# Performance work log

Measured on AMD Instinct MI355X. Metric: run time of the kernel, lower is better.

Reference implementation:

```python
import jax, jax.numpy as jnp
import numpy as np

N_NODES = 16
N_EDGES = 64
N_LAYERS = 4


def _gcn(x, src, dst, emask, W, b):
    # PyG GCNConv: add self-loops, symmetric deg^-1/2 normalization, sum-aggregate.
    n = x.shape[0]
    h = x @ W  # [n, d_out]
    deg = jax.ops.segment_sum(emask, dst, num_segments=n) + 1.0  # +1 self-loop
    dinv = jax.lax.rsqrt(deg)
    norm = dinv[src] * dinv[dst] * emask  # masked-out edges get 0 weight
    out = jax.ops.segment_sum(norm[:, None] * h[src], dst, num_segments=n)
    return out + (dinv * dinv)[:, None] * h + b  # self-loop term + bias


def _sag_pool(x, src, dst, emask, w_rel, b_rel, w_root, k):
    # SAGPooling with GraphConv scorer: score = lin_rel(sum_j x_j) + lin_root(x)
    n = x.shape[0]
    agg = jax.ops.segment_sum(emask[:, None] * x[src], dst, num_segments=n)
    score = agg @ w_rel + b_rel + x @ w_root  # [n]
    perm = jnp.argsort(-score)[:k]  # top-k nodes
    x_new = x[perm] * jnp.tanh(score[perm])[:, None]
    kept = jnp.zeros(n, bool).at[perm].set(True)
    pos = jnp.zeros(n, jnp.int32).at[perm].set(jnp.arange(k, dtype=jnp.int32))
    emask_new = emask * kept[src] * kept[dst]  # drop edges touching removed nodes
    return x_new, pos[src], pos[dst], emask_new


def _conv_gnn(x, src, dst, W0, Ws, bs, pWrel, pbrel, pWroot, linW, linb):
    emask = jnp.ones(src.shape[0], x.dtype)
    n = x.shape[0]
    for i in range(N_LAYERS):
        W = W0 if i == 0 else Ws[i - 1]
        x = jax.nn.relu(_gcn(x, src, dst, emask, W, bs[i]))
        k = -(-n // 2)  # ceil(0.5 * n) -- SAGPooling ratio=0.5
        x, src, dst, emask = _sag_pool(x, src, dst, emask, pWrel[i], pbrel[i], pWroot[i], k)
        n = k
    x = x @ linW + linb  # [1, 128]
    return jax.nn.log_softmax(x, axis=1)


def _fc(h, fcW, fcb, lnw, lnb):
    eps = 1e-5
    for i in range(3):
        h = h @ fcW[i] + fcb[i]
        mu = h.mean(-1, keepdims=True)
        var = ((h - mu) ** 2).mean(-1, keepdims=True)
        h = (h - mu) * jax.lax.rsqrt(var + eps) * lnw[i] + lnb[i]
        h = jax.nn.relu(h)
    return h @ fcW[3] + fcb[3]


def setup_inputs() -> dict:
    key = jax.random.key(0)
    ks = iter(jax.random.split(key, 64))

    def rn(shape, s=0.05):
        return jax.random.normal(next(ks), shape, jnp.float32) * s

    def gnn_params(p):
        return {
            p + '_W0': rn((45, 128)), p + '_W': rn((3, 128, 128)),
            p + '_b': jnp.zeros((4, 128), jnp.float32),
            p + '_pWrel': rn((4, 128)), p + '_pbrel': jnp.zeros((4,), jnp.float32),
            p + '_pWroot': rn((4, 128)),
            p + '_linW': rn((128, 128)), p + '_linb': jnp.zeros((128,), jnp.float32),
        }

    inp = {
        'gp_x': rn((N_NODES, 45), 1.0), 'sp_x': rn((N_NODES, 45), 1.0),
        'gp_src': jax.random.randint(next(ks), (N_EDGES,), 0, N_NODES, jnp.int32),
        'gp_dst': jax.random.randint(next(ks), (N_EDGES,), 0, N_NODES, jnp.int32),
        'sp_src': jax.random.randint(next(ks), (N_EDGES,), 0, N_NODES, jnp.int32),
        'sp_dst': jax.random.randint(next(ks), (N_EDGES,), 0, N_NODES, jnp.int32),
        'fcW': rn((4, 256, 256)), 'fcb': jnp.zeros((4, 256), jnp.float32),
        'lnw': jnp.ones((3, 256), jnp.float32), 'lnb': jnp.zeros((3, 256), jnp.float32),
    }
    inp.update(gnn_params('g'))
    inp.update(gnn_params('s'))
    return inp


def reference(gp_x, sp_x, gp_src, gp_dst, sp_src, sp_dst,
              g_W0, g_W, g_b, g_pWrel, g_pbrel, g_pWroot, g_linW, g_linb,
              s_W0, s_W, s_b, s_pWrel, s_pbrel, s_pWroot, s_linW, s_linb,
              fcW, fcb, lnw, lnb):
    out1 = _conv_gnn(gp_x, gp_src, gp_dst, g_W0, g_W, g_b, g_pWrel, g_pbrel, g_pWroot, g_linW, g_linb)
    out2 = _conv_gnn(sp_x, sp_src, sp_dst, s_W0, s_W, s_b, s_pWrel, s_pbrel, s_pWroot, s_linW, s_linb)
    concat = jnp.concatenate((out1.reshape(-1), out2.reshape(-1)))  # [256]
    return _fc(concat, fcW, fcb, lnw, lnb)
```

## Files before the change

### kernel.cpp

```cpp
#include <hip/hip_runtime.h>
#include <math.h>

#define MAGIC 0x5F3759DFu
typedef unsigned int u32;

__device__ __forceinline__ void bar_lds(){
  asm volatile("s_waitcnt lgkmcnt(0)\n\ts_barrier" ::: "memory");
}
__device__ __forceinline__ void bar_vm0(){
  asm volatile("s_waitcnt vmcnt(0) lgkmcnt(0)\n\ts_barrier" ::: "memory");
}
__device__ __forceinline__ void bar_vm8(){
  asm volatile("s_waitcnt vmcnt(8) lgkmcnt(0)\n\ts_barrier" ::: "memory");
}

__device__ inline float wsum(float v){
  #pragma unroll
  for (int o=32;o;o>>=1) v += __shfl_xor(v,o,64);
  return v;
}
__device__ inline float wmax(float v){
  #pragma unroll
  for (int o=32;o;o>>=1) v = fmaxf(v,__shfl_xor(v,o,64));
  return v;
}
__device__ inline float hsum32(float v){
  #pragma unroll
  for (int o=16;o;o>>=1) v += __shfl_xor(v,o,64);
  return v;
}
__device__ __forceinline__ void stageW(const float* g, float* l, int nfloats,
                                       int wid, int lane){
  const int nch = nfloats>>8;
  for (int c=wid; c<nch; c+=8)
    __builtin_amdgcn_global_load_lds(
      (__attribute__((address_space(1))) u32*)(void*)(g+(c<<8)+(lane<<2)),
      (__attribute__((address_space(3))) u32*)(void*)(l+(c<<8)), 16, 0, 0);
}
__device__ __forceinline__ void pf(const float* p, int nfloats, int tid){
  float4 acc={0.f,0.f,0.f,0.f};
  const int nq=nfloats>>2;
  for (int i=tid;i<nq;i+=512){
    const float4 v=((const float4*)p)[i];
    acc.x+=v.x; acc.y+=v.y; acc.z+=v.z; acc.w+=v.w;
  }
  asm volatile("" :: "v"(acc.x),"v"(acc.y),"v"(acc.z),"v"(acc.w));
}
__device__ __forceinline__ void poll1(const u32* f, int lane){
  u32 v=0;
  do {
    if (lane==0) v=__hip_atomic_load(f,__ATOMIC_ACQUIRE,__HIP_MEMORY_SCOPE_AGENT);
    v=(u32)__shfl((int)v,0,64);
    if (v!=MAGIC) __builtin_amdgcn_s_sleep(1);
  } while (v!=MAGIC);
}
__device__ __forceinline__ float aload(const float* p){
  return __hip_atomic_load(p,__ATOMIC_RELAXED,__HIP_MEMORY_SCOPE_AGENT);
}
__device__ __forceinline__ void astore(float* p, float v){
  __hip_atomic_store(p,v,__ATOMIC_RELAXED,__HIP_MEMORY_SCOPE_AGENT);
}

template<int F,int VH,int N>
__device__ __forceinline__ void cmain2(int lt, const float* slot,
                                       const float* ZBp, float* PBp){
  constexpr int CH = 128/F;
  const int c4 = lt&31, r = lt>>5;
  const int fh = r & (F-1), vh = r / F;
  const int f0 = fh*CH;
  const float4* slot4 = (const float4*)slot;
  float4 acc[VH];
  #pragma unroll
  for (int i=0;i<VH;++i) acc[i]=make_float4(0.f,0.f,0.f,0.f);
  #pragma unroll
  for (int f=0; f<CH; ++f){
    const float4 w4 = slot4[(f0+f)*32 + c4];
    #pragma unroll
    for (int i=0;i<VH;++i){
      const float zv = ZBp[((vh*VH+i)<<7) + f0 + f];
      acc[i].x+=zv*w4.x; acc[i].y+=zv*w4.y; acc[i].z+=zv*w4.z; acc[i].w+=zv*w4.w;
    }
  }
  #pragma unroll
  for (int i=0;i<VH;++i){
    acc[i].x+=__shfl_xor(acc[i].x,32,64);
    acc[i].y+=__shfl_xor(acc[i].y,32,64);
    acc[i].z+=__shfl_xor(acc[i].z,32,64);
    acc[i].w+=__shfl_xor(acc[i].w,32,64);
  }
  if (!(r&1)){
    const int fp = fh>>1;
    float4* P4=(float4*)PBp;
    #pragma unroll
    for (int i=0;i<VH;++i)
      P4[(fp*N + vh*VH + i)*32 + c4] = acc[i];
  }
}

__global__ __launch_bounds__(512,1) void net_kernel(
    const float* __restrict__ gp_x, const float* __restrict__ sp_x,
    const int* __restrict__ gp_src, const int* __restrict__ gp_dst,
    const int* __restrict__ sp_src, const int* __restrict__ sp_dst,
    const float* __restrict__ g_W0, const float* __restrict__ g_W,
    const float* __restrict__ g_b,  const float* __restrict__ g_pWrel,
    const float* __restrict__ g_pbrel, const float* __restrict__ g_pWroot,
    const float* __restrict__ g_linW, const float* __restrict__ g_linb,
    const float* __restrict__ s_W0, const float* __restrict__ s_W,
    const float* __restrict__ s_b,  const float* __restrict__ s_pWrel,
    const float* __restrict__ s_pbrel, const float* __restrict__ s_pWroot,
    const float* __restrict__ s_linW, const float* __restrict__ s_linb,
    const float* __restrict__ fcW, const float* __restrict__ fcb,
    const float* __restrict__ lnw, const float* __restrict__ lnb,
    float* __restrict__ wsbuf, float* __restrict__ out)
{
  __shared__ __align__(16) float slotA[16384];
  __shared__ __align__(16) float slotB[16384];
  __shared__ __align__(16) float XBx[16][128];
  __shared__ __align__(16) float ZBraw[1024];
  __shared__ __align__(16) float PBf[2048];
  __shared__ __align__(16) float wrelL[512], wrootL[512];
  __shared__ __align__(16) float Adn[256], Mdn[256];
  __shared__ float d1P[64], d2P[64];
  __shared__ float yA[128];
  __shared__ float tsA[8]; __shared__ int permA[8];
  __shared__ float fcin[256]; __shared__ float wpart[16];

  const int lt  = threadIdx.x;
  const int bid = blockIdx.x;
  const int wid = lt>>6, lane = lt&63;

  if (bid >= 6){
    if (bid==6){ pf(g_W0,5760,lt); pf(g_pWrel,512,lt); pf(g_pWroot,512,lt);
                 pf(g_b,512,lt);   pf(g_linb,128,lt); }
    else if (bid==7){ pf(s_W0,5760,lt); pf(s_pWrel,512,lt); pf(s_pWroot,512,lt);
                 pf(s_b,512,lt);   pf(s_linb,128,lt); }
    else if (bid<=11) pf(g_W + (bid-8)*12288, 12288, lt);
    else if (bid<=15) pf(s_W + (bid-12)*12288, 12288, lt);
    else if (bid<=17) pf(g_linW + (bid-16)*8192, 8192, lt);
    else              pf(s_linW + (bid-18)*8192, 8192, lt);
    return;
  }

  if (bid >= 2){
    const int L = bid-2;
    const int qfc=(wid<<3)+(lane&7), f0fc=(lane>>3)<<5;
    float4 wr[32];
    #pragma unroll
    for (int t=0;t<32;++t) wr[t]=*(const float4*)(fcW+(L<<16)+(f0fc+t)*256+(qfc<<2));
    const float4 bb=*(const float4*)(fcb+(L<<8)+(qfc<<2));
    float4 lw={0,0,0,0}, lb2={0,0,0,0};
    if (L<3){ lw=*(const float4*)(lnw+(L<<8)+(qfc<<2)); lb2=*(const float4*)(lnb+(L<<8)+(qfc<<2)); }

    float zr[32];
    if (L==0){
      poll1((const u32*)(wsbuf+128), lane);
      poll1((const u32*)(wsbuf+384), lane);
      if (lt<256){
        const float* src = wsbuf + (lt<128 ? lt : 128+lt);
        fcin[lt]=aload(src);
      }
      bar_lds();
      #pragma unroll
      for (int t=0;t<32;++t) zr[t]=fcin[f0fc+t];
    } else {
      const int floff = (L==1)?768 : (L==2)?1280 : 1792;
      const int srcoff= (L==1)?512 : (L==2)?1024 : 1536;
      poll1((const u32*)(wsbuf+floff), lane);
      #pragma unroll
      for (int t=0;t<32;++t) zr[t]=aload(wsbuf+srcoff+f0fc+t);
    }
    float4 a={0.f,0.f,0.f,0.f};
    #pragma unroll
    for (int t=0;t<32;++t){
      a.x+=zr[t]*wr[t].x; a.y+=zr[t]*wr[t].y; a.z+=zr[t]*wr[t].z; a.w+=zr[t]*wr[t].w;
    }
    #pragma unroll
    for (int m=8;m<64;m<<=1){
      a.x+=__shfl_xor(a.x,m,64); a.y+=__shfl_xor(a.y,m,64);
      a.z+=__shfl_xor(a.z,m,64); a.w+=__shfl_xor(a.w,m,64);
    }
    if (L==3){
      if (lane<8){
        float4 r; r.x=a.x+bb.x; r.y=a.y+bb.y; r.z=a.z+bb.z; r.w=a.w+bb.w;
        *(float4*)(out+(qfc<<2))=r;
      }
      return;
    }
    const bool act=(lane<8);
    float4 hv={0.f,0.f,0.f,0.f};
    if (act){
      hv.x=a.x+bb.x; hv.y=a.y+bb.y; hv.z=a.z+bb.z; hv.w=a.w+bb.w;
      float s=hv.x+hv.y+hv.z+hv.w;
      float s2=hv.x*hv.x+hv.y*hv.y+hv.z*hv.z+hv.w*hv.w;
      #pragma unroll
      for (int m=1;m<8;m<<=1){ s+=__shfl_xor(s,m,64); s2+=__shfl_xor(s2,m,64); }
      if (lane==0){ wpart[wid]=s; wpart[8+wid]=s2; }
    }
    bar_lds();
    if (act){
      float S=0.f,S2=0.f;
      #pragma unroll
      for (int w2=0;w2<8;++w2){ S+=wpart[w2]; S2+=wpart[8+w2]; }
      const float mu=S*(1.f/256.f);
      const float ri=rsqrtf(S2*(1.f/256.f)-mu*mu+1e-5f);
      float* dst=wsbuf+512+L*512+(qfc<<2);
      astore(dst+0,fmaxf((hv.x-mu)*ri*lw.x+lb2.x,0.f));
      astore(dst+1,fmaxf((hv.y-mu)*ri*lw.y+lb2.y,0.f));
      astore(dst+2,fmaxf((hv.z-mu)*ri*lw.z+lb2.z,0.f));
      astore(dst+3,fmaxf((hv.w-mu)*ri*lw.w+lb2.w,0.f));
    }
    bar_vm0();
    if (lt==0) __hip_atomic_store((u32*)(wsbuf+512+L*512+256),MAGIC,__ATOMIC_RELEASE,__HIP_MEMORY_SCOPE_AGENT);
    return;
  }

  const int br = bid;
  const float* x0    = br ? sp_x    : gp_x;
  const int*   srcg  = br ? sp_src  : gp_src;
  const int*   dstg  = br ? sp_dst  : gp_dst;
  const float* W0    = br ? s_W0    : g_W0;
  const float* Wl    = br ? s_W     : g_W;
  const float* bl    = br ? s_b     : g_b;
  const float* wrel  = br ? s_pWrel : g_pWrel;
  const float* brel  = br ? s_pbrel : g_pbrel;
  const float* wroot = br ? s_pWroot: g_pWroot;
  const float* linWg = br ? s_linW  : g_linW;
  const float* linb  = br ? s_linb  : g_linb;
  float* wsOut = wsbuf + br*256;
  u32*   wsFlag = (u32*)(wsbuf + 128 + br*256);

  float xv[4];
  #pragma unroll
  for (int r=0;r<4;++r){
    const int i=lt+(r<<9), v=i>>7, f=i&127;
    xv[r] = (f<45)? x0[v*45+f] : 0.f;
  }
  int es=0, ed=0; float emk=0.f;
  if (lt<64){ es=srcg[lt]; ed=dstg[lt]; emk=1.f; }
  const float4 brelv = *(const float4*)brel;
  const int bi4=(lt&31)<<2;
  const float4 blv0=*(const float4*)(bl       + bi4);
  const float4 blv1=*(const float4*)(bl + 128 + bi4);
  const float4 blv2=*(const float4*)(bl + 256 + bi4);
  const float4 blv3=*(const float4*)(bl + 384 + bi4);
  const float linb_s = linb[lt>>2];
  asm volatile("" ::: "memory");
  stageW(wrel,  wrelL,  512, wid, lane);
  stageW(wroot, wrootL, 512, wid, lane);
  stageW(Wl,    slotA, 16384, wid, lane);

  auto build_dense=[&](int kk, float wlane, bool with_ts){
    const float4 z4={0.f,0.f,0.f,0.f};
    *(float4*)&Adn[lt<<2]=z4;
    *(float4*)&Mdn[lt<<2]=z4;
    const bool act=(emk!=0.f);
    int mycnt=0;
    for (int v=0;v<kk;++v){
      const unsigned long long m=__ballot(act&&(ed==v));
      if (lt==v) mycnt=__popcll(m);
    }
    const float dinvl=rsqrtf(1.f+(float)mycnt);
    const float dvs=__shfl(dinvl,es,64);
    const float dvd=__shfl(dinvl,ed,64);
    if (act){
      atomicAdd(&Adn[ed*16+es], dvs*dvd*wlane);
      atomicAdd(&Mdn[ed*16+es], 1.f);
    }
    if (lt<kk){
      const float tv = with_ts ? tsA[lt] : 1.f;
      atomicAdd(&Adn[lt*17], dinvl*dinvl*tv);
    }
  };
  auto doE=[&](int n,int k,float bv,bool rebuild){
    if (lt<64){
      const float d1s=(lt<n)? d1P[lt<<2] : 0.f;
      float sc=-INFINITY;
      if (lt<n){
        float acc=d2P[lt<<2]+bv;
        for (int u=0;u<n;++u) acc += Mdn[lt*16+u]*__shfl(d1s,u,64);
        sc=acc;
      }
      int rank=0;
      for (int u=0;u<n;++u){
        const float su=__shfl(sc,u,64);
        rank += (su>sc || (su==sc && u<lt)) ? 1:0;
      }
      const int kept=(lt<n && rank<k)?1:0;
      const int pos=kept?rank:0;
      const float tval=kept?tanhf(sc):0.f;
      if (kept){ permA[rank]=lt; tsA[rank]=tval; }
      const float ts_src=__shfl(tval,es,64);
      const int ks=__shfl(kept,es,64), kd=__shfl(kept,ed,64);
      const int ps=__shfl(pos,es,64),  pd=__shfl(pos,ed,64);
      emk *= (float)(ks&kd);
      es=ps; ed=pd;
      if (rebuild) build_dense(k, ts_src, true);
    }
  };
  auto doB=[&](int n){
    if (lt<(n<<5)){
      const int v=lt>>5, j4=(lt&31)<<2;
      float4 a={0.f,0.f,0.f,0.f};
      for (int u=0;u<n;++u){
        const float w=Adn[v*16+u];
        const float4 xs=*(const float4*)&XBx[permA[u]][j4];
        a.x+=w*xs.x; a.y+=w*xs.y; a.z+=w*xs.z; a.w+=w*xs.w;
      }
      *(float4*)&ZBraw[(v<<7)+j4]=a;
    }
  };
  auto creduce2=[&](int F, int N, int L, float4 bl4){
    if (lt < (N<<5)){
      const int v=lt>>5, c4=lt&31;
      const float4* P4=(const float4*)PBf;
      float4 acc=bl4;
      for (int fp=0; fp<(F>>1); ++fp){
        const float4 p=P4[(fp*N+v)*32+c4];
        acc.x+=p.x; acc.y+=p.y; acc.z+=p.z; acc.w+=p.w;
      }
      float4 o;
      o.x=fmaxf(acc.x,0.f); o.y=fmaxf(acc.y,0.f);
      o.z=fmaxf(acc.z,0.f); o.w=fmaxf(acc.w,0.f);
      *(float4*)&XBx[v][c4<<2]=o;
      const float4 wr4=*(const float4*)&wrelL[(L<<7)+(c4<<2)];
      const float4 wo4=*(const float4*)&wrootL[(L<<7)+(c4<<2)];
      float p1=o.x*wr4.x+o.y*wr4.y+o.z*wr4.z+o.w*wr4.w;
      float p2=o.x*wo4.x+o.y*wo4.y+o.z*wo4.z+o.w*wo4.w;
      p1=hsum32(p1); p2=hsum32(p2);
      if ((lane&31)==0){ d1P[v<<2]=p1; d2P[v<<2]=p2; }
    }
  };

  #pragma unroll
  for (int r=0;r<4;++r){
    const int i=lt+(r<<9), v=i>>7, f=i&127;
    XBx[v][f]=xv[r];
  }
  if (lt<64) build_dense(16, 1.f, false);
  bar_lds();

  if (lt<256){
    const int v=lt>>4, j4=(lt&15)<<2;
    if (j4<48){
      float4 a={0.f,0.f,0.f,0.f};
      for (int u=0;u<16;++u){
        const float w=Adn[v*16+u];
        const float4 xs=*(const float4*)&XBx[u][j4];
        a.x+=w*xs.x; a.y+=w*xs.y; a.z+=w*xs.z; a.w+=w*xs.w;
      }
      *(float4*)&ZBraw[v*48+j4]=a;
    }
  }
  bar_vm8();

  {
    const int v=lt>>5, c4=lt&31, j4=c4<<2;
    const float* zrow=&ZBraw[v*48];
    float4 a={0.f,0.f,0.f,0.f};
    #pragma unroll
    for (int bb=0;bb<2;++bb){
      float4 wr[16]; float zr[16];
      #pragma unroll
      for (int t=0;t<16;++t){ wr[t]=*(const float4*)(W0+(bb*16+t)*128+j4); zr[t]=zrow[bb*16+t]; }
      #pragma unroll
      for (int t=0;t<16;++t){ a.x+=zr[t]*wr[t].x; a.y+=zr[t]*wr[t].y; a.z+=zr[t]*wr[t].z; a.w+=zr[t]*wr[t].w; }
    }
    { float4 wr[13]; float zr[13];
      #pragma unroll
      for (int t=0;t<13;++t){ wr[t]=*(const float4*)(W0+(32+t)*128+j4); zr[t]=zrow[32+t]; }
      #pragma unroll
      for (int t=0;t<13;++t){ a.x+=zr[t]*wr[t].x; a.y+=zr[t]*wr[t].y; a.z+=zr[t]*wr[t].z; a.w+=zr[t]*wr[t].w; }
    }
    float4 ox;
    ox.x=fmaxf(a.x+blv0.x,0.f); ox.y=fmaxf(a.y+blv0.y,0.f);
    ox.z=fmaxf(a.z+blv0.z,0.f); ox.w=fmaxf(a.w+blv0.w,0.f);
    *(float4*)&XBx[v][j4]=ox;
    const float4 wr4=*(const float4*)&wrelL[j4];
    const float4 wo4=*(const float4*)&wrootL[j4];
    float p1=ox.x*wr4.x+ox.y*wr4.y+ox.z*wr4.z+ox.w*wr4.w;
    float p2=ox.x*wo4.x+ox.y*wo4.y+ox.z*wo4.z+ox.w*wo4.w;
    p1=hsum32(p1); p2=hsum32(p2);
    if ((lane&31)==0){
      const int vv=(wid<<1)|(lane>>5);
      d1P[vv<<2]=p1; d2P[vv<<2]=p2;
    }
  }
  stageW(Wl+16384, slotB, 16384, wid, lane);
  bar_lds();

  doE(16, 8, brelv.x, true);    bar_lds();
  doB(8);                       bar_vm8();
  cmain2<4,2,8>(lt, slotA, ZBraw, PBf);  bar_lds();
  creduce2(4, 8, 1, blv1);      bar_lds();
  stageW(Wl+32768, slotA, 16384, wid, lane);
  doE(8, 4, brelv.y, true);     bar_lds();
  doB(4);                       bar_vm8();
  cmain2<8,2,4>(lt, slotB, ZBraw, PBf); bar_lds();
  creduce2(8, 4, 2, blv2);      bar_lds();
  stageW(linWg, slotB, 16384, wid, lane);
  doE(4, 2, brelv.z, true);     bar_lds();
  doB(2);                       bar_vm8();
  cmain2<8,1,2>(lt, slotA, ZBraw, PBf); bar_lds();
  creduce2(8, 2, 3, blv3);      bar_lds();
  doE(2, 1, brelv.w, false);    bar_vm0();

  {
    const int oj=lt>>2, fh=lt&3;
    const int prow=permA[0];
    float p=0.f;
    #pragma unroll
    for (int i=0;i<32;++i){
      const int f=(fh<<5)+i;
      p += XBx[prow][f]*slotB[f*128+oj];
    }
    p+=__shfl_xor(p,1,64); p+=__shfl_xor(p,2,64);
    if (fh==0) yA[oj]=p*tsA[0]+linb_s;
  }
  bar_lds();
  if (lt<128){
    const int ln=lt&63;
    const float a0=yA[ln], b0=yA[64+ln];
    const float m=wmax(fmaxf(a0,b0));
    const float sum=wsum(expf(a0-m)+expf(b0-m));
    const float lse=m+logf(sum);
    astore(&wsOut[lt], yA[lt]-lse);
  }
  bar_vm0();
  if (lt==0) __hip_atomic_store(wsFlag, MAGIC, __ATOMIC_RELEASE, __HIP_MEMORY_SCOPE_AGENT);
}

extern "C" void kernel_launch(void* const* d_in, const int* in_sizes, int n_in,
                              void* d_out, int out_size, void* d_ws, size_t ws_size,
                              hipStream_t stream){
  net_kernel<<<20,512,0,stream>>>(
    (const float*)d_in[0],(const float*)d_in[1],
    (const int*)d_in[2],(const int*)d_in[3],(const int*)d_in[4],(const int*)d_in[5],
    (const float*)d_in[10],(const float*)d_in[11],(const float*)d_in[12],(const float*)d_in[13],
    (const float*)d_in[14],(const float*)d_in[15],(const float*)d_in[16],(const float*)d_in[17],
    (const float*)d_in[18],(const float*)d_in[19],(const float*)d_in[20],(const float*)d_in[21],
    (const float*)d_in[22],(const float*)d_in[23],(const float*)d_in[24],(const float*)d_in[25],
    (const float*)d_in[6],(const float*)d_in[7],(const float*)d_in[8],(const float*)d_in[9],
    (float*)d_ws,(float*)d_out);
}
```

Before: 24.17 us.

## Fuse first FC layer into GNN branch blocks and replace final pooling with closed form

Each GNN branch block now computes its half of the first FC matmul (128 input features against its slice of fcW[0]) from register-prefetched weights. It writes a partial result, and the FC layer-0 block only sums the two partials, adds the bias and applies LayerNorm, which removes one dependent cross-block stage. The last SAG pooling step (2 nodes to 1) is replaced by a direct comparison of two scores and a tanh, instead of calling doE plus a barrier. The grid shrinks by one block. In exchange the branch blocks hold more registers and the workspace offsets and flags are remapped.

```diff
diff --git a/kernel.cpp b/kernel.cpp
--- a/kernel.cpp
+++ b/kernel.cpp
@@ -128,22 +128,23 @@
   const int lt  = threadIdx.x;
   const int bid = blockIdx.x;
   const int wid = lt>>6, lane = lt&63;
-
-  if (bid >= 6){
-    if (bid==6){ pf(g_W0,5760,lt); pf(g_pWrel,512,lt); pf(g_pWroot,512,lt);
+  const int qfc = (wid<<3)+(lane&7);
+
+  if (bid >= 5){
+    if (bid==5){ pf(g_W0,5760,lt); pf(g_pWrel,512,lt); pf(g_pWroot,512,lt);
                  pf(g_b,512,lt);   pf(g_linb,128,lt); }
-    else if (bid==7){ pf(s_W0,5760,lt); pf(s_pWrel,512,lt); pf(s_pWroot,512,lt);
+    else if (bid==6){ pf(s_W0,5760,lt); pf(s_pWrel,512,lt); pf(s_pWroot,512,lt);
                  pf(s_b,512,lt);   pf(s_linb,128,lt); }
-    else if (bid<=11) pf(g_W + (bid-8)*12288, 12288, lt);
-    else if (bid<=15) pf(s_W + (bid-12)*12288, 12288, lt);
-    else if (bid<=17) pf(g_linW + (bid-16)*8192, 8192, lt);
-    else              pf(s_linW + (bid-18)*8192, 8192, lt);
+    else if (bid<=10) pf(g_W + (bid-7)*12288, 12288, lt);
+    else if (bid<=14) pf(s_W + (bid-11)*12288, 12288, lt);
+    else if (bid<=16) pf(g_linW + (bid-15)*8192, 8192, lt);
+    else              pf(s_linW + (bid-17)*8192, 8192, lt);
     return;
   }
 
   if (bid >= 2){
-    const int L = bid-2;
-    const int qfc=(wid<<3)+(lane&7), f0fc=(lane>>3)<<5;
+    const int L = bid-1;
+    const int f0fc=(lane>>3)<<5;
     float4 wr[32];
     #pragma unroll
     for (int t=0;t<32;++t) wr[t]=*(const float4*)(fcW+(L<<16)+(f0fc+t)*256+(qfc<<2));
@@ -152,19 +153,31 @@
     if (L<3){ lw=*(const float4*)(lnw+(L<<8)+(qfc<<2)); lb2=*(const float4*)(lnb+(L<<8)+(qfc<<2)); }
 
     float zr[32];
-    if (L==0){
-      poll1((const u32*)(wsbuf+128), lane);
-      poll1((const u32*)(wsbuf+384), lane);
+    if (bid==2){
+      float b0=0.f,w0=0.f,l0=0.f;
+      if (lt<256){ b0=fcb[lt]; w0=lnw[lt]; l0=lnb[lt]; }
+      poll1((const u32*)(wsbuf+256), lane);
+      poll1((const u32*)(wsbuf+576), lane);
+      float h=0.f;
       if (lt<256){
-        const float* src = wsbuf + (lt<128 ? lt : 128+lt);
-        fcin[lt]=aload(src);
+        h = aload(wsbuf+lt) + aload(wsbuf+320+lt) + b0;
+        float s=wsum(h), s2=wsum(h*h);
+        if (lane==0){ wpart[wid]=s; wpart[8+wid]=s2; }
+      }
+      bar_lds();
+      if (lt<256){
+        const float S =wpart[0]+wpart[1]+wpart[2]+wpart[3];
+        const float S2=wpart[8]+wpart[9]+wpart[10]+wpart[11];
+        const float mu=S*(1.f/256.f);
+        const float ri=rsqrtf(S2*(1.f/256.f)-mu*mu+1e-5f);
+        fcin[lt]=fmaxf((h-mu)*ri*w0+l0,0.f);
       }
       bar_lds();
       #pragma unroll
       for (int t=0;t<32;++t) zr[t]=fcin[f0fc+t];
     } else {
-      const int floff = (L==1)?768 : (L==2)?1280 : 1792;
-      const int srcoff= (L==1)?512 : (L==2)?1024 : 1536;
+      const int floff = (bid==3)?896:1216;
+      const int srcoff= (bid==3)?640:960;
       poll1((const u32*)(wsbuf+floff), lane);
       #pragma unroll
       for (int t=0;t<32;++t) zr[t]=aload(wsbuf+srcoff+f0fc+t);
@@ -179,7 +192,7 @@
       a.x+=__shfl_xor(a.x,m,64); a.y+=__shfl_xor(a.y,m,64);
       a.z+=__shfl_xor(a.z,m,64); a.w+=__shfl_xor(a.w,m,64);
     }
-    if (L==3){
+    if (bid==4){
       if (lane<8){
         float4 r; r.x=a.x+bb.x; r.y=a.y+bb.y; r.z=a.z+bb.z; r.w=a.w+bb.w;
         *(float4*)(out+(qfc<<2))=r;
@@ -203,14 +216,14 @@
       for (int w2=0;w2<8;++w2){ S+=wpart[w2]; S2+=wpart[8+w2]; }
       const float mu=S*(1.f/256.f);
       const float ri=rsqrtf(S2*(1.f/256.f)-mu*mu+1e-5f);
-      float* dst=wsbuf+512+L*512+(qfc<<2);
+      float* dst=wsbuf + ((bid==2)?640:960) + (qfc<<2);
       astore(dst+0,fmaxf((hv.x-mu)*ri*lw.x+lb2.x,0.f));
       astore(dst+1,fmaxf((hv.y-mu)*ri*lw.y+lb2.y,0.f));
       astore(dst+2,fmaxf((hv.z-mu)*ri*lw.z+lb2.z,0.f));
       astore(dst+3,fmaxf((hv.w-mu)*ri*lw.w+lb2.w,0.f));
     }
     bar_vm0();
-    if (lt==0) __hip_atomic_store((u32*)(wsbuf+512+L*512+256),MAGIC,__ATOMIC_RELEASE,__HIP_MEMORY_SCOPE_AGENT);
+    if (lt==0) __hip_atomic_store((u32*)(wsbuf+((bid==2)?896:1216)),MAGIC,__ATOMIC_RELEASE,__HIP_MEMORY_SCOPE_AGENT);
     return;
   }
 
@@ -226,8 +239,9 @@
   const float* wroot = br ? s_pWroot: g_pWroot;
   const float* linWg = br ? s_linW  : g_linW;
   const float* linb  = br ? s_linb  : g_linb;
-  float* wsOut = wsbuf + br*256;
-  u32*   wsFlag = (u32*)(wsbuf + 128 + br*256);
+  float* wsOut = wsbuf + br*320;
+  u32*   wsFlag = (u32*)(wsbuf + 256 + br*320);
+  const int f0fc=(lane>>3)<<4;
 
   float xv[4];
   #pragma unroll
@@ -385,6 +399,11 @@
       d1P[vv<<2]=p1; d2P[vv<<2]=p2;
     }
   }
+  float4 wfc[16];
+  #pragma unroll
+  for (int t=0;t<16;++t)
+    wfc[t]=*(const float4*)(fcW + ((br<<7)+f0fc+t)*256 + (qfc<<2));
+  asm volatile("" ::: "memory");
   stageW(Wl+16384, slotB, 16384, wid, lane);
   bar_lds();
 
@@ -401,12 +420,15 @@
   doE(4, 2, brelv.z, true);     bar_lds();
   doB(2);                       bar_vm8();
   cmain2<8,1,2>(lt, slotA, ZBraw, PBf); bar_lds();
-  creduce2(8, 2, 3, blv3);      bar_lds();
-  doE(2, 1, brelv.w, false);    bar_vm0();
+  creduce2(8, 2, 3, blv3);      bar_vm0();
 
   {
+    const float bv=brelv.w;
+    const float s0v = d2P[0]+bv + Mdn[0] *d1P[0] + Mdn[1] *d1P[4];
+    const float s1v = d2P[4]+bv + Mdn[16]*d1P[0] + Mdn[17]*d1P[4];
+    const int   prow = (s1v>s0v) ? 1 : 0;
+    const float tsf  = tanhf(prow ? s1v : s0v);
     const int oj=lt>>2, fh=lt&3;
-    const int prow=permA[0];
     float p=0.f;
     #pragma unroll
     for (int i=0;i<32;++i){
@@ -414,7 +436,7 @@
       p += XBx[prow][f]*slotB[f*128+oj];
     }
     p+=__shfl_xor(p,1,64); p+=__shfl_xor(p,2,64);
-    if (fh==0) yA[oj]=p*tsA[0]+linb_s;
+    if (fh==0) yA[oj]=p*tsf+linb_s;
   }
   bar_lds();
   if (lt<128){
@@ -423,7 +445,25 @@
     const float m=wmax(fmaxf(a0,b0));
     const float sum=wsum(expf(a0-m)+expf(b0-m));
     const float lse=m+logf(sum);
-    astore(&wsOut[lt], yA[lt]-lse);
+    fcin[lt]=yA[lt]-lse;
+  }
+  bar_lds();
+  {
+    float4 a={0.f,0.f,0.f,0.f};
+    #pragma unroll
+    for (int t=0;t<16;++t){
+      const float zv=fcin[f0fc+t];
+      a.x+=zv*wfc[t].x; a.y+=zv*wfc[t].y; a.z+=zv*wfc[t].z; a.w+=zv*wfc[t].w;
+    }
+    #pragma unroll
+    for (int m=8;m<64;m<<=1){
+      a.x+=__shfl_xor(a.x,m,64); a.y+=__shfl_xor(a.y,m,64);
+      a.z+=__shfl_xor(a.z,m,64); a.w+=__shfl_xor(a.w,m,64);
+    }
+    if (lane<8){
+      float* dst=wsOut+(qfc<<2);
+      astore(dst+0,a.x); astore(dst+1,a.y); astore(dst+2,a.z); astore(dst+3,a.w);
+    }
   }
   bar_vm0();
   if (lt==0) __hip_atomic_store(wsFlag, MAGIC, __ATOMIC_RELEASE, __HIP_MEMORY_SCOPE_AGENT);
@@ -432,7 +472,7 @@
 extern "C" void kernel_launch(void* const* d_in, const int* in_sizes, int n_in,
                               void* d_out, int out_size, void* d_ws, size_t ws_size,
                               hipStream_t stream){
-  net_kernel<<<20,512,0,stream>>>(
+  net_kernel<<<19,512,0,stream>>>(
     (const float*)d_in[0],(const float*)d_in[1],
     (const int*)d_in[2],(const int*)d_in[3],(const int*)d_in[4],(const int*)d_in[5],
     (const float*)d_in[10],(const float*)d_in[11],(const float*)d_in[12],(const float*)d_in[13],
```

Result: no change. 24.18 us (+0.0%).
